# Kernel tuning notes

Measured on AMD Instinct MI355X. Metric: run time of the kernel, lower is better.

## Reference

```python
import jax, jax.numpy as jnp
import numpy as np

B, I, H = 16384, 512, 512
HH = H // 2


def _lrelu(v):
    return jnp.where(v > 0, v, 0.01 * v)


def setup_inputs() -> dict:
    key = jax.random.key(0)
    ks = jax.random.split(key, 20)
    s = 1.0 / np.sqrt(H)
    rn = lambda k, shp, sc: (jax.random.normal(k, shp, jnp.float32) * sc)
    return {
        "x": rn(ks[0], (B, I), 1.0),
        "h0": rn(ks[1], (1, B, H), 1.0),
        "c0": rn(ks[2], (1, B, H), 1.0),
        "cum": jax.random.uniform(ks[3], (B, 1), jnp.float32),
        # LSTM params (torch gate order i, f, g, o)
        "W_ih": rn(ks[4], (4 * H, I), s),
        "W_hh": rn(ks[5], (4 * H, H), s),
        "b_ih": rn(ks[6], (4 * H,), s),
        "b_hh": rn(ks[7], (4 * H,), s),
        # skip gate MLP
        "W_sp": rn(ks[8], (HH, H), s),
        "b_sp": rn(ks[9], (HH,), s),
        "W_sc": rn(ks[10], (HH, H), s),
        "b_sc": rn(ks[11], (HH,), s),
        "W_so": rn(ks[12], (1, HH), s),
        "b_so": rn(ks[13], (1,), s),
        # threshold gate MLP
        "W_tp": rn(ks[14], (HH, H), s),
        "b_tp": rn(ks[15], (HH,), s),
        "W_to": rn(ks[16], (1, HH), s),
        "b_to": rn(ks[17], (1,), s),
    }


def reference(x, h0, c0, cum, W_ih, W_hh, b_ih, b_hh,
              W_sp, b_sp, W_sc, b_sc, W_so, b_so,
              W_tp, b_tp, W_to, b_to):
    # single-step, single-layer LSTM
    gates = x @ W_ih.T + b_ih + h0[0] @ W_hh.T + b_hh  # [B, 4H]
    i_g, f_g, g_g, o_g = jnp.split(gates, 4, axis=-1)
    i_g = jax.nn.sigmoid(i_g)
    f_g = jax.nn.sigmoid(f_g)
    g_g = jnp.tanh(g_g)
    o_g = jax.nn.sigmoid(o_g)
    c1l = f_g * c0[0] + i_g * g_g          # [B, H]
    h1l = o_g * jnp.tanh(c1l)              # [B, H]
    h1, c1 = h1l[None], c1l[None]          # [1, B, H]

    # skip gate: delta prob from c0[-1], c1[-1]
    sg = _lrelu(c0[-1] @ W_sp.T + b_sp + c1[-1] @ W_sc.T + b_sc)  # [B, H/2]
    update_prob_delta = jax.nn.sigmoid(sg @ W_so.T + b_so)        # [B, 1]

    # threshold gate from c0[-1]
    tg = _lrelu(c0[-1] @ W_tp.T + b_tp)                           # [B, H/2]
    update_threshold = jax.nn.sigmoid(tg @ W_to.T + b_to)         # [B, 1]

    update_prob = cum + jnp.minimum(update_prob_delta, 1.0 - cum)  # [B, 1]
    # straight-through round: fwd hard threshold, bwd identity to prob
    hard = (update_prob > update_threshold).astype(jnp.float32)
    update_gate = update_prob + jax.lax.stop_gradient(hard - update_prob)

    new_h = update_gate * h1 + (1.0 - update_gate) * h0  # [1, B, H]
    new_c = update_gate * c1 + (1.0 - update_gate) * c0  # [1, B, H]
    update_cum = (1.0 - update_gate) * update_prob        # [B, 1]
    return (new_h, new_c, update_cum, update_prob_delta, update_prob)
```

## Files before the change

kernel.cpp:

```cpp
#include <hip/hip_runtime.h>
#include <math.h>

#define BB 16384
#define HH 512

typedef short short8 __attribute__((ext_vector_type(8)));
typedef float f32x4 __attribute__((ext_vector_type(4)));
typedef unsigned short ushort_t;

__device__ __forceinline__ float sigm(float v){ return 1.0f/(1.0f+expf(-v)); }

__device__ __forceinline__ unsigned short f2bf(float f){
    unsigned int u = __float_as_uint(f);
    u = u + 0x7FFFu + ((u>>16)&1u);
    return (unsigned short)(u>>16);
}
__device__ __forceinline__ float bf2f(unsigned short h){
    return __uint_as_float(((unsigned int)h)<<16);
}
__device__ __forceinline__ void gll16(const void* g, void* l){
    __builtin_amdgcn_global_load_lds((const __attribute__((address_space(1))) void*)g,
                                     (__attribute__((address_space(3))) void*)l, 16, 0, 0);
}
__device__ __forceinline__ void split_store(float v, ushort_t* ph, ushort_t* pl, int j){
    unsigned short h = f2bf(v);
    unsigned short l = f2bf(v - bf2f(h));
    ph[j] = h; pl[j] = l;
}

__global__ void k_prep_all(
    const float* __restrict__ x, const float* __restrict__ h0, const float* __restrict__ c0,
    const float* __restrict__ W_ih, const float* __restrict__ W_hh,
    const float* __restrict__ b_ih, const float* __restrict__ b_hh,
    const float* __restrict__ W_sp, const float* __restrict__ W_sc, const float* __restrict__ W_tp,
    const float* __restrict__ b_sp, const float* __restrict__ b_sc, const float* __restrict__ b_tp,
    ushort_t* __restrict__ A1h, ushort_t* __restrict__ A1l,
    ushort_t* __restrict__ A2h, ushort_t* __restrict__ A2l,
    ushort_t* __restrict__ B1h, ushort_t* __restrict__ B1l,
    ushort_t* __restrict__ B2h, ushort_t* __restrict__ B2l,
    float* __restrict__ bgp, float* __restrict__ bs2)
{
    int bid = blockIdx.x;
    if (bid < 8192) {
        int u = bid*256 + threadIdx.x;
        int r  = u & 255;
        int c  = (u >> 8) & 3;
        int kt = (u >> 10) & 31;
        int tm = u >> 15;
        int row = tm*256 + r;
        int k0 = kt*32 + c*8;
        const float* src = (k0 < 512) ? (x + (size_t)row*512 + k0)
                                      : (h0 + (size_t)row*512 + (k0-512));
        float4 v0 = *(const float4*)(src);
        float4 v1 = *(const float4*)(src+4);
        float vv[8] = {v0.x,v0.y,v0.z,v0.w,v1.x,v1.y,v1.z,v1.w};
        size_t off = (size_t)u * 8;
#pragma unroll
        for (int j=0;j<8;++j) split_store(vv[j], A1h+off, A1l+off, j);
    } else if (bid < 12288) {
        int u = (bid-8192)*256 + threadIdx.x;
        int r  = u & 127;
        int c  = (u >> 7) & 3;
        int tk = (u >> 9) & 15;
        int tm = u >> 13;
        int row = tm*128 + r;
        int k0 = tk*32 + c*8;
        const float* src = c0 + (size_t)row*512 + k0;
        float4 v0 = *(const float4*)(src);
        float4 v1 = *(const float4*)(src+4);
        float vv[8] = {v0.x,v0.y,v0.z,v0.w,v1.x,v1.y,v1.z,v1.w};
        size_t off = ((size_t)tm*32 + tk)*4096 + (size_t)(c*128 + r)*8;
#pragma unroll
        for (int j=0;j<8;++j) split_store(vv[j], A2h+off, A2l+off, j);
    } else if (bid < 13312) {
        int u = (bid-12288)*256 + threadIdx.x;
        int r  = u & 255;
        int c  = (u >> 8) & 3;
        int kt = (u >> 10) & 31;
        int tn = u >> 15;
        int g = (r>>4)&3;
        int h = tn*64 + (r>>6)*16 + (r&15);
        int wrow = g*512 + h;
        int k0 = kt*32 + c*8;
        const float* src = (k0 < 512) ? (W_ih + (size_t)wrow*512 + k0)
                                      : (W_hh + (size_t)wrow*512 + (k0-512));
        float4 v0 = *(const float4*)(src);
        float4 v1 = *(const float4*)(src+4);
        float vv[8] = {v0.x,v0.y,v0.z,v0.w,v1.x,v1.y,v1.z,v1.w};
        size_t off = (size_t)u * 8;
#pragma unroll
        for (int j=0;j<8;++j) split_store(vv[j], B1h+off, B1l+off, j);
        if (kt == 0 && c == 0) bgp[tn*256 + r] = b_ih[wrow] + b_hh[wrow];
    } else {
        int u = (bid-13312)*256 + threadIdx.x;
        int r  = u & 127;
        int c  = (u >> 7) & 3;
        int tk = (u >> 9) & 31;
        int tn = u >> 14;
        int n = tn*128 + r;
        int k0 = tk*32 + c*8;
        float vv[8];
        if (n < 256) {
            const float* src = (k0 < 512) ? (W_sp + (size_t)n*512 + k0)
                                          : (W_sc + (size_t)n*512 + (k0-512));
            float4 v0 = *(const float4*)(src);
            float4 v1 = *(const float4*)(src+4);
            vv[0]=v0.x; vv[1]=v0.y; vv[2]=v0.z; vv[3]=v0.w;
            vv[4]=v1.x; vv[5]=v1.y; vv[6]=v1.z; vv[7]=v1.w;
        } else if (k0 < 512) {
            const float* src = W_tp + (size_t)(n-256)*512 + k0;
            float4 v0 = *(const float4*)(src);
            float4 v1 = *(const float4*)(src+4);
            vv[0]=v0.x; vv[1]=v0.y; vv[2]=v0.z; vv[3]=v0.w;
            vv[4]=v1.x; vv[5]=v1.y; vv[6]=v1.z; vv[7]=v1.w;
        } else {
#pragma unroll
            for (int j=0;j<8;++j) vv[j] = 0.0f;
        }
        size_t off = (size_t)u * 8;
#pragma unroll
        for (int j=0;j<8;++j) split_store(vv[j], B2h+off, B2l+off, j);
        if (tk == 0 && c == 0) bs2[n] = (n < 256) ? (b_sp[n] + b_sc[n]) : b_tp[n-256];
    }
}

#define GSTEP(T, CA, CB, NA, NB, DO_READS, DO_STAGE, VMASM)                          \
  {                                                                                  \
    if (DO_READS) {                                                                  \
        const ushort_t* bufA1 = &lds[((T)+1) & 3][0];                                \
        const ushort_t* bufB1 = &lds[((T)+1) & 3][8192];                             \
        _Pragma("unroll") for (int f = 0; f < 8; ++f)                                \
            NA[f] = *(const short8*)&bufA1[aoff[f]];                                 \
        _Pragma("unroll") for (int f = 0; f < 4; ++f)                                \
            NB[f] = *(const short8*)&bufB1[boff[f]];                                 \
    }                                                                                \
    if (DO_STAGE) {                                                                  \
        const int uu = (T) + 3;                                                      \
        const ushort_t* As_ = ((uu >> 5) == 1) ? Al : Ah;                            \
        const ushort_t* Bs_ = ((uu >> 5) == 2) ? Bl : Bh;                            \
        size_t ga = ((size_t)tm*32 + (uu & 31))*8192 + (size_t)tid*8;                \
        size_t gb = ((size_t)tn*32 + (uu & 31))*8192 + (size_t)tid*8;                \
        ushort_t* dA = &lds[uu & 3][0];                                              \
        ushort_t* dB = &lds[uu & 3][8192];                                           \
        gll16(As_ + ga,        dA + tid*8);                                          \
        gll16(As_ + ga + 4096, dA + 4096 + tid*8);                                   \
        gll16(Bs_ + gb,        dB + tid*8);                                          \
        gll16(Bs_ + gb + 4096, dB + 4096 + tid*8);                                   \
    }                                                                                \
    __builtin_amdgcn_sched_barrier(0);                                               \
    __builtin_amdgcn_s_setprio(1);                                                   \
    _Pragma("unroll") for (int fm = 0; fm < 8; ++fm)                                 \
        _Pragma("unroll") for (int fn = 0; fn < 4; ++fn)                             \
            acc[fm][fn] = __builtin_amdgcn_mfma_f32_16x16x32_bf16(CA[fm], CB[fn], acc[fm][fn], 0,0,0); \
    __builtin_amdgcn_s_setprio(0);                                                   \
    asm volatile("s_waitcnt lgkmcnt(0)" ::: "memory");                               \
    __builtin_amdgcn_sched_barrier(0);                                               \
    VMASM;                                                                           \
    asm volatile("s_barrier" ::: "memory");                                          \
  }

__global__ __launch_bounds__(512, 2) void k_gemm_gates(
    const ushort_t* __restrict__ Ah, const ushort_t* __restrict__ Al,
    const ushort_t* __restrict__ Bh, const ushort_t* __restrict__ Bl,
    const float* __restrict__ bgp, const float* __restrict__ c0,
    float* __restrict__ outH, float* __restrict__ outC,
    ushort_t* __restrict__ A2h, ushort_t* __restrict__ A2l)
{
    __shared__ __align__(16) ushort_t lds[4][16384];
    const int tid  = threadIdx.x;
    const int lane = tid & 63;
    const int wid  = tid >> 6;
    const int wr   = wid >> 2;
    const int wc   = wid & 3;
    const int l15  = lane & 15;
    const int lq   = lane >> 4;
    const int bid  = (int)blockIdx.x;
    const int v    = (bid & 7)*64 + (bid >> 3);
    const int tm   = v >> 3;
    const int tn   = v & 7;

    f32x4 acc[8][4];
#pragma unroll
    for (int fn = 0; fn < 4; ++fn) {
        float bv = bgp[tn*256 + wc*64 + fn*16 + l15];
#pragma unroll
        for (int fm = 0; fm < 8; ++fm) {
            acc[fm][fn][0]=bv; acc[fm][fn][1]=bv; acc[fm][fn][2]=bv; acc[fm][fn][3]=bv;
        }
    }

    int aoff[8], boff[4];
#pragma unroll
    for (int f = 0; f < 8; ++f) aoff[f] = (lq*256 + wr*128 + f*16 + l15) * 8;
#pragma unroll
    for (int f = 0; f < 4; ++f) boff[f] = (lq*256 + wc*64 + f*16 + l15) * 8;

    short8 a0[8], b0[4], a1[8], b1[4];

#pragma unroll
    for (int u0 = 0; u0 < 3; ++u0) {
        size_t ga = ((size_t)tm*32 + u0)*8192 + (size_t)tid*8;
        size_t gb = ((size_t)tn*32 + u0)*8192 + (size_t)tid*8;
        gll16(Ah + ga,        &lds[u0][0]     + tid*8);
        gll16(Ah + ga + 4096, &lds[u0][4096]  + tid*8);
        gll16(Bh + gb,        &lds[u0][8192]  + tid*8);
        gll16(Bh + gb + 4096, &lds[u0][12288] + tid*8);
    }
    asm volatile("s_waitcnt vmcnt(4)" ::: "memory");
    asm volatile("s_barrier" ::: "memory");
#pragma unroll
    for (int f = 0; f < 8; ++f) a0[f] = *(const short8*)&lds[0][aoff[f]];
#pragma unroll
    for (int f = 0; f < 4; ++f) b0[f] = *(const short8*)&lds[0][8192 + boff[f]];
    asm volatile("s_waitcnt lgkmcnt(0)" ::: "memory");
    __builtin_amdgcn_sched_barrier(0);

    for (int t = 0; t < 92; t += 2) {
        GSTEP(t,   a0, b0, a1, b1, 1, 1, asm volatile("s_waitcnt vmcnt(4)" ::: "memory"));
        GSTEP(t+1, a1, b1, a0, b0, 1, 1, asm volatile("s_waitcnt vmcnt(4)" ::: "memory"));
    }
    GSTEP(92, a0, b0, a1, b1, 1, 1, asm volatile("s_waitcnt vmcnt(4)" ::: "memory"));
    GSTEP(93, a1, b1, a0, b0, 1, 0, asm volatile("s_waitcnt vmcnt(0)" ::: "memory"));
    GSTEP(94, a0, b0, a1, b1, 1, 0, ((void)0));
    GSTEP(95, a1, b1, a0, b0, 0, 0, ((void)0));

    const int h = tn*64 + wc*16 + l15;
#pragma unroll
    for (int fm = 0; fm < 8; ++fm) {
        int row0 = tm*256 + wr*128 + fm*16 + lq*4;
#pragma unroll
        for (int r = 0; r < 4; ++r) {
            int row = row0 + r;
            size_t idx = (size_t)row*512 + h;
            float ig = sigm(acc[fm][0][r]);
            float fg = sigm(acc[fm][1][r]);
            float gg = tanhf(acc[fm][2][r]);
            float og = sigm(acc[fm][3][r]);
            float c1 = fg*c0[idx] + ig*gg;
            float h1 = og*tanhf(c1);
            outC[idx] = c1;
            outH[idx] = h1;
            unsigned short ch = f2bf(c1);
            unsigned short cl = f2bf(c1 - bf2f(ch));
            size_t a2 = ((size_t)(row>>7)*32 + 16 + (h>>5))*4096
                      + (size_t)((((h>>3)&3))*128 + (row&127))*8 + (h&7);
            A2h[a2] = ch;
            A2l[a2] = cl;
        }
    }
}

#define SSTEP(T, CA, CB, NA, NB, DO_READS, DO_STAGE, VMASM)                          \
  {                                                                                  \
    if (DO_READS) {                                                                  \
        const ushort_t* bufA1 = &lds2[((T)+1) & 3][0];                               \
        const ushort_t* bufB1 = &lds2[((T)+1) & 3][4096];                            \
        _Pragma("unroll") for (int f = 0; f < 4; ++f)                                \
            NA[f] = *(const short8*)&bufA1[aoff[f]];                                 \
        _Pragma("unroll") for (int f = 0; f < 4; ++f)                                \
            NB[f] = *(const short8*)&bufB1[boff[f]];                                 \
    }                                                                                \
    if (DO_STAGE) {                                                                  \
        const int uu = (T) + 3;                                                      \
        const ushort_t* As_ = ((uu >> 5) == 1) ? Al : Ah;                            \
        const ushort_t* Bs_ = ((uu >> 5) == 2) ? Bl : Bh;                            \
        size_t ga = ((size_t)tm*32 + (uu & 31))*4096 + (size_t)tid*8;                \
        size_t gb = ((size_t)tn*32 + (uu & 31))*4096 + (size_t)tid*8;                \
        ushort_t* dA = &lds2[uu & 3][0];                                             \
        ushort_t* dB = &lds2[uu & 3][4096];                                          \
        gll16(As_ + ga,        dA + tid*8);                                          \
        gll16(As_ + ga + 2048, dA + 2048 + tid*8);                                   \
        gll16(Bs_ + gb,        dB + tid*8);                                          \
        gll16(Bs_ + gb + 2048, dB + 2048 + tid*8);                                   \
    }                                                                                \
    __builtin_amdgcn_sched_barrier(0);                                               \
    __builtin_amdgcn_s_setprio(1);                                                   \
    _Pragma("unroll") for (int fm = 0; fm < 4; ++fm)                                 \
        _Pragma("unroll") for (int fn = 0; fn < 4; ++fn)                             \
            acc[fm][fn] = __builtin_amdgcn_mfma_f32_16x16x32_bf16(CA[fm], CB[fn], acc[fm][fn], 0,0,0); \
    __builtin_amdgcn_s_setprio(0);                                                   \
    asm volatile("s_waitcnt lgkmcnt(0)" ::: "memory");                               \
    __builtin_amdgcn_sched_barrier(0);                                               \
    VMASM;                                                                           \
    asm volatile("s_barrier" ::: "memory");                                          \
  }

__global__ __launch_bounds__(256, 2) void k_gemm_sgtg(
    const ushort_t* __restrict__ Ah, const ushort_t* __restrict__ Al,
    const ushort_t* __restrict__ Bh, const ushort_t* __restrict__ Bl,
    const float* __restrict__ bs2,
    float* __restrict__ sgtg)
{
    __shared__ __align__(16) ushort_t lds2[4][8192];
    const int tid  = threadIdx.x;
    const int lane = tid & 63;
    const int wid  = tid >> 6;
    const int wr   = wid >> 1;
    const int wc   = wid & 1;
    const int l15  = lane & 15;
    const int lq   = lane >> 4;
    const int bid  = (int)blockIdx.x;
    const int v    = (bid & 7)*64 + (bid >> 3);
    const int tm   = v >> 2;
    const int tn   = v & 3;

    f32x4 acc[4][4];
#pragma unroll
    for (int fn = 0; fn < 4; ++fn) {
        float bv = bs2[tn*128 + wc*64 + fn*16 + l15];
#pragma unroll
        for (int fm = 0; fm < 4; ++fm) {
            acc[fm][fn][0]=bv; acc[fm][fn][1]=bv; acc[fm][fn][2]=bv; acc[fm][fn][3]=bv;
        }
    }

    int aoff[4], boff[4];
#pragma unroll
    for (int f = 0; f < 4; ++f) {
        aoff[f] = (lq*128 + wr*64 + f*16 + l15) * 8;
        boff[f] = (lq*128 + wc*64 + f*16 + l15) * 8;
    }

    short8 a0[4], b0[4], a1[4], b1[4];

#pragma unroll
    for (int u0 = 0; u0 < 3; ++u0) {
        size_t ga = ((size_t)tm*32 + u0)*4096 + (size_t)tid*8;
        size_t gb = ((size_t)tn*32 + u0)*4096 + (size_t)tid*8;
        gll16(Ah + ga,        &lds2[u0][0]    + tid*8);
        gll16(Ah + ga + 2048, &lds2[u0][2048] + tid*8);
        gll16(Bh + gb,        &lds2[u0][4096] + tid*8);
        gll16(Bh + gb + 2048, &lds2[u0][6144] + tid*8);
    }
    asm volatile("s_waitcnt vmcnt(4)" ::: "memory");
    asm volatile("s_barrier" ::: "memory");
#pragma unroll
    for (int f = 0; f < 4; ++f) a0[f] = *(const short8*)&lds2[0][aoff[f]];
#pragma unroll
    for (int f = 0; f < 4; ++f) b0[f] = *(const short8*)&lds2[0][4096 + boff[f]];
    asm volatile("s_waitcnt lgkmcnt(0)" ::: "memory");
    __builtin_amdgcn_sched_barrier(0);

    for (int t = 0; t < 92; t += 2) {
        SSTEP(t,   a0, b0, a1, b1, 1, 1, asm volatile("s_waitcnt vmcnt(4)" ::: "memory"));
        SSTEP(t+1, a1, b1, a0, b0, 1, 1, asm volatile("s_waitcnt vmcnt(4)" ::: "memory"));
    }
    SSTEP(92, a0, b0, a1, b1, 1, 1, asm volatile("s_waitcnt vmcnt(4)" ::: "memory"));
    SSTEP(93, a1, b1, a0, b0, 1, 0, asm volatile("s_waitcnt vmcnt(0)" ::: "memory"));
    SSTEP(94, a0, b0, a1, b1, 1, 0, ((void)0));
    SSTEP(95, a1, b1, a0, b0, 0, 0, ((void)0));

#pragma unroll
    for (int fm = 0; fm < 4; ++fm) {
        int row0 = tm*128 + wr*64 + fm*16 + lq*4;
#pragma unroll
        for (int fn = 0; fn < 4; ++fn) {
            int n = tn*128 + wc*64 + fn*16 + l15;
#pragma unroll
            for (int r = 0; r < 4; ++r) {
                int row = row0 + r;
                float vv = acc[fm][fn][r];
                vv = vv > 0.f ? vv : 0.01f*vv;
                sgtg[(size_t)row*512 + n] = vv;
            }
        }
    }
}

__global__ __launch_bounds__(256) void k_final(
    const float* __restrict__ sgtg,
    const float* __restrict__ h0, const float* __restrict__ c0,
    const float* __restrict__ cum,
    const float* __restrict__ W_so, const float* __restrict__ b_so,
    const float* __restrict__ W_to, const float* __restrict__ b_to,
    float* __restrict__ outH, float* __restrict__ outC,
    float* __restrict__ outCum, float* __restrict__ outDelta, float* __restrict__ outProb)
{
    int w = threadIdx.x >> 6;
    int lane = threadIdx.x & 63;
    int b = blockIdx.x * 4 + w;
    const float* row = sgtg + (size_t)b * 512;
    float so = 0.f, to = 0.f;
#pragma unroll
    for (int u = 0; u < 4; ++u) {
        int c = lane + 64 * u;
        so = fmaf(row[c], W_so[c], so);
        to = fmaf(row[256 + c], W_to[c], to);
    }
#pragma unroll
    for (int off = 32; off; off >>= 1) {
        so += __shfl_down(so, off);
        to += __shfl_down(to, off);
    }
    so = __shfl(so, 0);
    to = __shfl(to, 0);
    float delta = sigm(so + b_so[0]);
    float thr   = sigm(to + b_to[0]);
    float cu = cum[b];
    float prob = cu + fminf(delta, 1.0f - cu);
    float hard = (prob > thr) ? 1.0f : 0.0f;
    if (lane == 0) {
        outDelta[b] = delta;
        outProb[b]  = prob;
        outCum[b]   = (1.0f - hard) * prob;
    }
    if (hard == 0.0f) {
#pragma unroll
        for (int u = 0; u < 8; ++u) {
            size_t idx = (size_t)b * 512 + lane + 64 * u;
            outH[idx] = h0[idx];
            outC[idx] = c0[idx];
        }
    }
}

extern "C" void kernel_launch(void* const* d_in, const int* in_sizes, int n_in,
                              void* d_out, int out_size, void* d_ws, size_t ws_size,
                              hipStream_t stream)
{
    const float* x    = (const float*)d_in[0];
    const float* h0   = (const float*)d_in[1];
    const float* c0   = (const float*)d_in[2];
    const float* cum  = (const float*)d_in[3];
    const float* W_ih = (const float*)d_in[4];
    const float* W_hh = (const float*)d_in[5];
    const float* b_ih = (const float*)d_in[6];
    const float* b_hh = (const float*)d_in[7];
    const float* W_sp = (const float*)d_in[8];
    const float* b_sp = (const float*)d_in[9];
    const float* W_sc = (const float*)d_in[10];
    const float* b_sc = (const float*)d_in[11];
    const float* W_so = (const float*)d_in[12];
    const float* b_so = (const float*)d_in[13];
    const float* W_tp = (const float*)d_in[14];
    const float* b_tp = (const float*)d_in[15];
    const float* W_to = (const float*)d_in[16];
    const float* b_to = (const float*)d_in[17];

    float* out      = (float*)d_out;
    float* outH     = out;
    float* outC     = out + (size_t)BB * HH;
    float* outCum   = out + (size_t)2 * BB * HH;
    float* outDelta = outCum + BB;
    float* outProb  = outDelta + BB;

    char* w = (char*)d_ws;
    ushort_t* A1h = (ushort_t*)(w);
    ushort_t* A1l = (ushort_t*)(w + 33554432ull);
    ushort_t* A2h = (ushort_t*)(w + 67108864ull);
    ushort_t* A2l = (ushort_t*)(w + 100663296ull);
    ushort_t* B1h = (ushort_t*)(w + 134217728ull);
    ushort_t* B1l = (ushort_t*)(w + 138412032ull);
    ushort_t* B2h = (ushort_t*)(w + 142606336ull);
    ushort_t* B2l = (ushort_t*)(w + 143654912ull);
    float*    bgp = (float*)(w + 144703488ull);
    float*    bs2 = (float*)(w + 144711680ull);
    float*    sgtg = (float*)A1h;

    k_prep_all<<<13568, 256, 0, stream>>>(x, h0, c0, W_ih, W_hh, b_ih, b_hh,
                                          W_sp, W_sc, W_tp, b_sp, b_sc, b_tp,
                                          A1h, A1l, A2h, A2l, B1h, B1l, B2h, B2l,
                                          bgp, bs2);
    k_gemm_gates<<<512, 512, 0, stream>>>(A1h, A1l, B1h, B1l, bgp, c0,
                                          outH, outC, A2h, A2l);
    k_gemm_sgtg<<<512, 256, 0, stream>>>(A2h, A2l, B2h, B2l, bs2, sgtg);
    k_final<<<4096, 256, 0, stream>>>(sgtg, h0, c0, cum, W_so, b_so, W_to, b_to,
                                      outH, outC, outCum, outDelta, outProb);
}
```

Baseline: 340.0 us.

## Load A operand directly from global in MFMA fragment layout, stage only B in LDS

```diff
diff --git a/kernel.cpp b/kernel.cpp
--- a/kernel.cpp
+++ b/kernel.cpp
@@ -43,12 +43,14 @@
     int bid = blockIdx.x;
     if (bid < 8192) {
         int u = bid*256 + threadIdx.x;
-        int r  = u & 255;
-        int c  = (u >> 8) & 3;
-        int kt = (u >> 10) & 31;
-        int tm = u >> 15;
-        int row = tm*256 + r;
-        int k0 = kt*32 + c*8;
+        int tm  = u >> 14;
+        int rem = u & 16383;
+        int kt  = rem >> 9;
+        int lq  = (rem >> 7) & 3;
+        int f   = (rem >> 4) & 7;
+        int l15 = rem & 15;
+        int row = tm*128 + f*16 + l15;
+        int k0  = kt*32 + lq*8;
         const float* src = (k0 < 512) ? (x + (size_t)row*512 + k0)
                                       : (h0 + (size_t)row*512 + (k0-512));
         float4 v0 = *(const float4*)(src);
@@ -59,17 +61,19 @@
         for (int j=0;j<8;++j) split_store(vv[j], A1h+off, A1l+off, j);
     } else if (bid < 12288) {
         int u = (bid-8192)*256 + threadIdx.x;
-        int r  = u & 127;
-        int c  = (u >> 7) & 3;
-        int tk = (u >> 9) & 15;
-        int tm = u >> 13;
-        int row = tm*128 + r;
-        int k0 = tk*32 + c*8;
+        int tm  = u >> 13;
+        int rem = u & 8191;
+        int kt  = rem >> 9;
+        int lq  = (rem >> 7) & 3;
+        int f   = (rem >> 4) & 7;
+        int l15 = rem & 15;
+        int row = tm*128 + f*16 + l15;
+        int k0  = kt*32 + lq*8;
         const float* src = c0 + (size_t)row*512 + k0;
         float4 v0 = *(const float4*)(src);
         float4 v1 = *(const float4*)(src+4);
         float vv[8] = {v0.x,v0.y,v0.z,v0.w,v1.x,v1.y,v1.z,v1.w};
-        size_t off = ((size_t)tm*32 + tk)*4096 + (size_t)(c*128 + r)*8;
+        size_t off = ((size_t)tm*32 + kt)*4096 + (size_t)(rem & 511)*8;
 #pragma unroll
         for (int j=0;j<8;++j) split_store(vv[j], A2h+off, A2l+off, j);
     } else if (bid < 13312) {
@@ -124,60 +128,57 @@
     }
 }
 
-#define GSTEP(T, CA, CB, NA, NB, DO_READS, DO_STAGE, VMASM)                          \
+#define GSTEP(T, CA, CB, NA, NB, DO_A, DO_BSTAGE, DO_BREAD, WAITASM)                 \
   {                                                                                  \
-    if (DO_READS) {                                                                  \
-        const ushort_t* bufA1 = &lds[((T)+1) & 3][0];                                \
-        const ushort_t* bufB1 = &lds[((T)+1) & 3][8192];                             \
+    if (DO_A) {                                                                      \
+        const int un = (T) + 1;                                                      \
+        const ushort_t* As_ = ((un >> 5) == 1) ? Al : Ah;                            \
+        const ushort_t* ap = As_ + ((size_t)tm*32 + (un & 31))*4096 + aG;            \
         _Pragma("unroll") for (int f = 0; f < 8; ++f)                                \
-            NA[f] = *(const short8*)&bufA1[aoff[f]];                                 \
-        _Pragma("unroll") for (int f = 0; f < 4; ++f)                                \
-            NB[f] = *(const short8*)&bufB1[boff[f]];                                 \
-    }                                                                                \
-    if (DO_STAGE) {                                                                  \
+            NA[f] = *(const short8*)(ap + f*128);                                    \
+    }                                                                                \
+    if (DO_BSTAGE) {                                                                 \
         const int uu = (T) + 3;                                                      \
-        const ushort_t* As_ = ((uu >> 5) == 1) ? Al : Ah;                            \
         const ushort_t* Bs_ = ((uu >> 5) == 2) ? Bl : Bh;                            \
-        size_t ga = ((size_t)tm*32 + (uu & 31))*8192 + (size_t)tid*8;                \
-        size_t gb = ((size_t)tn*32 + (uu & 31))*8192 + (size_t)tid*8;                \
-        ushort_t* dA = &lds[uu & 3][0];                                              \
-        ushort_t* dB = &lds[uu & 3][8192];                                           \
-        gll16(As_ + ga,        dA + tid*8);                                          \
-        gll16(As_ + ga + 4096, dA + 4096 + tid*8);                                   \
-        gll16(Bs_ + gb,        dB + tid*8);                                          \
-        gll16(Bs_ + gb + 4096, dB + 4096 + tid*8);                                   \
-    }                                                                                \
-    __builtin_amdgcn_sched_barrier(0);                                               \
+        const ushort_t* gB = Bs_ + ((size_t)tn*32 + (uu & 31))*8192;                 \
+        ushort_t* dB = &ldsB[uu & 3][0];                                             \
+        _Pragma("unroll") for (int q = 0; q < 4; ++q)                                \
+            gll16(gB + (q*256 + tid)*8, dB + (q*256 + tid)*8);                       \
+    }                                                                                \
+    if (DO_BREAD) {                                                                  \
+        const ushort_t* bB = &ldsB[((T)+1) & 3][0];                                  \
+        _Pragma("unroll") for (int fn = 0; fn < 4; ++fn)                             \
+            NB[fn] = *(const short8*)&bB[boff[fn]];                                  \
+    }                                                                                \
     __builtin_amdgcn_s_setprio(1);                                                   \
     _Pragma("unroll") for (int fm = 0; fm < 8; ++fm)                                 \
         _Pragma("unroll") for (int fn = 0; fn < 4; ++fn)                             \
             acc[fm][fn] = __builtin_amdgcn_mfma_f32_16x16x32_bf16(CA[fm], CB[fn], acc[fm][fn], 0,0,0); \
     __builtin_amdgcn_s_setprio(0);                                                   \
-    asm volatile("s_waitcnt lgkmcnt(0)" ::: "memory");                               \
     __builtin_amdgcn_sched_barrier(0);                                               \
-    VMASM;                                                                           \
+    WAITASM;                                                                         \
+    __builtin_amdgcn_sched_barrier(0);                                               \
     asm volatile("s_barrier" ::: "memory");                                          \
   }
 
-__global__ __launch_bounds__(512, 2) void k_gemm_gates(
+__global__ __launch_bounds__(256, 2) void k_gemm_gates(
     const ushort_t* __restrict__ Ah, const ushort_t* __restrict__ Al,
     const ushort_t* __restrict__ Bh, const ushort_t* __restrict__ Bl,
     const float* __restrict__ bgp, const float* __restrict__ c0,
     float* __restrict__ outH, float* __restrict__ outC,
     ushort_t* __restrict__ A2h, ushort_t* __restrict__ A2l)
 {
-    __shared__ __align__(16) ushort_t lds[4][16384];
+    __shared__ __align__(16) ushort_t ldsB[4][8192];
     const int tid  = threadIdx.x;
     const int lane = tid & 63;
-    const int wid  = tid >> 6;
-    const int wr   = wid >> 2;
-    const int wc   = wid & 3;
+    const int wc   = tid >> 6;
     const int l15  = lane & 15;
     const int lq   = lane >> 4;
     const int bid  = (int)blockIdx.x;
-    const int v    = (bid & 7)*64 + (bid >> 3);
+    const int v    = (bid & 7)*128 + (bid >> 3);
     const int tm   = v >> 3;
     const int tn   = v & 7;
+    const int aG   = lq*1024 + l15*8;
 
     f32x4 acc[8][4];
 #pragma unroll
@@ -189,45 +190,44 @@
         }
     }
 
-    int aoff[8], boff[4];
-#pragma unroll
-    for (int f = 0; f < 8; ++f) aoff[f] = (lq*256 + wr*128 + f*16 + l15) * 8;
+    int boff[4];
 #pragma unroll
     for (int f = 0; f < 4; ++f) boff[f] = (lq*256 + wc*64 + f*16 + l15) * 8;
 
     short8 a0[8], b0[4], a1[8], b1[4];
 
-#pragma unroll
-    for (int u0 = 0; u0 < 3; ++u0) {
-        size_t ga = ((size_t)tm*32 + u0)*8192 + (size_t)tid*8;
-        size_t gb = ((size_t)tn*32 + u0)*8192 + (size_t)tid*8;
-        gll16(Ah + ga,        &lds[u0][0]     + tid*8);
-        gll16(Ah + ga + 4096, &lds[u0][4096]  + tid*8);
-        gll16(Bh + gb,        &lds[u0][8192]  + tid*8);
-        gll16(Bh + gb + 4096, &lds[u0][12288] + tid*8);
+    {
+        const ushort_t* ap0 = Ah + (size_t)tm*32*4096 + aG;
+#pragma unroll
+        for (int f = 0; f < 8; ++f) a0[f] = *(const short8*)(ap0 + f*128);
+#pragma unroll
+        for (int u0 = 0; u0 < 3; ++u0) {
+            const ushort_t* gB = Bh + ((size_t)tn*32 + u0)*8192;
+#pragma unroll
+            for (int q = 0; q < 4; ++q)
+                gll16(gB + (q*256 + tid)*8, &ldsB[u0][(q*256 + tid)*8]);
+        }
     }
     asm volatile("s_waitcnt vmcnt(4)" ::: "memory");
     asm volatile("s_barrier" ::: "memory");
 #pragma unroll
-    for (int f = 0; f < 8; ++f) a0[f] = *(const short8*)&lds[0][aoff[f]];
-#pragma unroll
-    for (int f = 0; f < 4; ++f) b0[f] = *(const short8*)&lds[0][8192 + boff[f]];
+    for (int f = 0; f < 4; ++f) b0[f] = *(const short8*)&ldsB[0][boff[f]];
     asm volatile("s_waitcnt lgkmcnt(0)" ::: "memory");
     __builtin_amdgcn_sched_barrier(0);
 
     for (int t = 0; t < 92; t += 2) {
-        GSTEP(t,   a0, b0, a1, b1, 1, 1, asm volatile("s_waitcnt vmcnt(4)" ::: "memory"));
-        GSTEP(t+1, a1, b1, a0, b0, 1, 1, asm volatile("s_waitcnt vmcnt(4)" ::: "memory"));
-    }
-    GSTEP(92, a0, b0, a1, b1, 1, 1, asm volatile("s_waitcnt vmcnt(4)" ::: "memory"));
-    GSTEP(93, a1, b1, a0, b0, 1, 0, asm volatile("s_waitcnt vmcnt(0)" ::: "memory"));
-    GSTEP(94, a0, b0, a1, b1, 1, 0, ((void)0));
-    GSTEP(95, a1, b1, a0, b0, 0, 0, ((void)0));
+        GSTEP(t,   a0,b0, a1,b1, 1,1,1, asm volatile("s_waitcnt vmcnt(4) lgkmcnt(0)" ::: "memory"));
+        GSTEP(t+1, a1,b1, a0,b0, 1,1,1, asm volatile("s_waitcnt vmcnt(4) lgkmcnt(0)" ::: "memory"));
+    }
+    GSTEP(92, a0,b0, a1,b1, 1,1,1, asm volatile("s_waitcnt vmcnt(4) lgkmcnt(0)" ::: "memory"));
+    GSTEP(93, a1,b1, a0,b0, 1,0,1, asm volatile("s_waitcnt vmcnt(0) lgkmcnt(0)" ::: "memory"));
+    GSTEP(94, a0,b0, a1,b1, 1,0,1, asm volatile("s_waitcnt vmcnt(0) lgkmcnt(0)" ::: "memory"));
+    GSTEP(95, a1,b1, a0,b0, 0,0,0, ((void)0));
 
     const int h = tn*64 + wc*16 + l15;
 #pragma unroll
     for (int fm = 0; fm < 8; ++fm) {
-        int row0 = tm*256 + wr*128 + fm*16 + lq*4;
+        int row0 = tm*128 + fm*16 + lq*4;
 #pragma unroll
         for (int r = 0; r < 4; ++r) {
             int row = row0 + r;
@@ -243,119 +243,115 @@
             unsigned short ch = f2bf(c1);
             unsigned short cl = f2bf(c1 - bf2f(ch));
             size_t a2 = ((size_t)(row>>7)*32 + 16 + (h>>5))*4096
-                      + (size_t)((((h>>3)&3))*128 + (row&127))*8 + (h&7);
+                      + (size_t)((h>>3)&3)*1024 + (size_t)(((row&127)>>4))*128
+                      + (size_t)(row&15)*8 + (h&7);
             A2h[a2] = ch;
             A2l[a2] = cl;
         }
     }
 }
 
-#define SSTEP(T, CA, CB, NA, NB, DO_READS, DO_STAGE, VMASM)                          \
+#define SSTEP(T, CA, CB, NA, NB, DO_A, DO_BSTAGE, DO_BREAD, WAITASM)                 \
   {                                                                                  \
-    if (DO_READS) {                                                                  \
-        const ushort_t* bufA1 = &lds2[((T)+1) & 3][0];                               \
-        const ushort_t* bufB1 = &lds2[((T)+1) & 3][4096];                            \
-        _Pragma("unroll") for (int f = 0; f < 4; ++f)                                \
-            NA[f] = *(const short8*)&bufA1[aoff[f]];                                 \
-        _Pragma("unroll") for (int f = 0; f < 4; ++f)                                \
-            NB[f] = *(const short8*)&bufB1[boff[f]];                                 \
-    }                                                                                \
-    if (DO_STAGE) {                                                                  \
+    if (DO_A) {                                                                      \
+        const int un = (T) + 1;                                                      \
+        const ushort_t* As_ = ((un >> 5) == 1) ? Al : Ah;                            \
+        const ushort_t* ap = As_ + ((size_t)tm*32 + (un & 31))*4096 + aG;            \
+        _Pragma("unroll") for (int f = 0; f < 8; ++f)                                \
+            NA[f] = *(const short8*)(ap + f*128);                                    \
+    }                                                                                \
+    if (DO_BSTAGE) {                                                                 \
         const int uu = (T) + 3;                                                      \
-        const ushort_t* As_ = ((uu >> 5) == 1) ? Al : Ah;                            \
         const ushort_t* Bs_ = ((uu >> 5) == 2) ? Bl : Bh;                            \
-        size_t ga = ((size_t)tm*32 + (uu & 31))*4096 + (size_t)tid*8;                \
-        size_t gb = ((size_t)tn*32 + (uu & 31))*4096 + (size_t)tid*8;                \
-        ushort_t* dA = &lds2[uu & 3][0];                                             \
-        ushort_t* dB = &lds2[uu & 3][4096];                                          \
-        gll16(As_ + ga,        dA + tid*8);                                          \
-        gll16(As_ + ga + 2048, dA + 2048 + tid*8);                                   \
-        gll16(Bs_ + gb,        dB + tid*8);                                          \
-        gll16(Bs_ + gb + 2048, dB + 2048 + tid*8);                                   \
-    }                                                                                \
-    __builtin_amdgcn_sched_barrier(0);                                               \
+        const ushort_t* gB = Bs_ + ((size_t)tn*32 + (uu & 31))*4096;                 \
+        ushort_t* dB = &ldsB2[uu & 3][0];                                            \
+        _Pragma("unroll") for (int q = 0; q < 2; ++q)                                \
+            gll16(gB + (q*256 + tid)*8, dB + (q*256 + tid)*8);                       \
+    }                                                                                \
+    if (DO_BREAD) {                                                                  \
+        const ushort_t* bB = &ldsB2[((T)+1) & 3][0];                                 \
+        _Pragma("unroll") for (int fn = 0; fn < 2; ++fn)                             \
+            NB[fn] = *(const short8*)&bB[boff2[fn]];                                 \
+    }                                                                                \
     __builtin_amdgcn_s_setprio(1);                                                   \
-    _Pragma("unroll") for (int fm = 0; fm < 4; ++fm)                                 \
-        _Pragma("unroll") for (int fn = 0; fn < 4; ++fn)                             \
+    _Pragma("unroll") for (int fm = 0; fm < 8; ++fm)                                 \
+        _Pragma("unroll") for (int fn = 0; fn < 2; ++fn)                             \
             acc[fm][fn] = __builtin_amdgcn_mfma_f32_16x16x32_bf16(CA[fm], CB[fn], acc[fm][fn], 0,0,0); \
     __builtin_amdgcn_s_setprio(0);                                                   \
-    asm volatile("s_waitcnt lgkmcnt(0)" ::: "memory");                               \
     __builtin_amdgcn_sched_barrier(0);                                               \
-    VMASM;                                                                           \
+    WAITASM;                                                                         \
+    __builtin_amdgcn_sched_barrier(0);                                               \
     asm volatile("s_barrier" ::: "memory");                                          \
   }
 
-__global__ __launch_bounds__(256, 2) void k_gemm_sgtg(
+__global__ __launch_bounds__(256, 3) void k_gemm_sgtg(
     const ushort_t* __restrict__ Ah, const ushort_t* __restrict__ Al,
     const ushort_t* __restrict__ Bh, const ushort_t* __restrict__ Bl,
     const float* __restrict__ bs2,
     float* __restrict__ sgtg)
 {
-    __shared__ __align__(16) ushort_t lds2[4][8192];
+    __shared__ __align__(16) ushort_t ldsB2[4][4096];
     const int tid  = threadIdx.x;
     const int lane = tid & 63;
-    const int wid  = tid >> 6;
-    const int wr   = wid >> 1;
-    const int wc   = wid & 1;
+    const int wc   = tid >> 6;
     const int l15  = lane & 15;
     const int lq   = lane >> 4;
     const int bid  = (int)blockIdx.x;
     const int v    = (bid & 7)*64 + (bid >> 3);
     const int tm   = v >> 2;
     const int tn   = v & 3;
-
-    f32x4 acc[4][4];
-#pragma unroll
-    for (int fn = 0; fn < 4; ++fn) {
-        float bv = bs2[tn*128 + wc*64 + fn*16 + l15];
-#pragma unroll
-        for (int fm = 0; fm < 4; ++fm) {
+    const int aG   = lq*1024 + l15*8;
+
+    f32x4 acc[8][2];
+#pragma unroll
+    for (int fn = 0; fn < 2; ++fn) {
+        float bv = bs2[tn*128 + wc*32 + fn*16 + l15];
+#pragma unroll
+        for (int fm = 0; fm < 8; ++fm) {
             acc[fm][fn][0]=bv; acc[fm][fn][1]=bv; acc[fm][fn][2]=bv; acc[fm][fn][3]=bv;
         }
     }
 
-    int aoff[4], boff[4];
-#pragma unroll
-    for (int f = 0; f < 4; ++f) {
-        aoff[f] = (lq*128 + wr*64 + f*16 + l15) * 8;
-        boff[f] = (lq*128 + wc*64 + f*16 + l15) * 8;
-    }
-
-    short8 a0[4], b0[4], a1[4], b1[4];
-
-#pragma unroll
-    for (int u0 = 0; u0 < 3; ++u0) {
-        size_t ga = ((size_t)tm*32 + u0)*4096 + (size_t)tid*8;
-        size_t gb = ((size_t)tn*32 + u0)*4096 + (size_t)tid*8;
-        gll16(Ah + ga,        &lds2[u0][0]    + tid*8);
-        gll16(Ah + ga + 2048, &lds2[u0][2048] + tid*8);
-        gll16(Bh + gb,        &lds2[u0][4096] + tid*8);
-        gll16(Bh + gb + 2048, &lds2[u0][6144] + tid*8);
-    }
-    asm volatile("s_waitcnt vmcnt(4)" ::: "memory");
+    int boff2[2];
+#pragma unroll
+    for (int f = 0; f < 2; ++f) boff2[f] = (lq*128 + wc*32 + f*16 + l15) * 8;
+
+    short8 a0[8], b0[2], a1[8], b1[2];
+
+    {
+        const ushort_t* ap0 = Ah + (size_t)tm*32*4096 + aG;
+#pragma unroll
+        for (int f = 0; f < 8; ++f) a0[f] = *(const short8*)(ap0 + f*128);
+#pragma unroll
+        for (int u0 = 0; u0 < 3; ++u0) {
+            const ushort_t* gB = Bh + ((size_t)tn*32 + u0)*4096;
+#pragma unroll
+            for (int q = 0; q < 2; ++q)
+                gll16(gB + (q*256 + tid)*8, &ldsB2[u0][(q*256 + tid)*8]);
+        }
+    }
+    asm volatile("s_waitcnt vmcnt(2)" ::: "memory");
     asm volatile("s_barrier" ::: "memory");
 #pragma unroll
-    for (int f = 0; f < 4; ++f) a0[f] = *(const short8*)&lds2[0][aoff[f]];
-#pragma unroll
-    for (int f = 0; f < 4; ++f) b0[f] = *(const short8*)&lds2[0][4096 + boff[f]];
+    for (int f = 0; f < 2; ++f) b0[f] = *(const short8*)&ldsB2[0][boff2[f]];
     asm volatile("s_waitcnt lgkmcnt(0)" ::: "memory");
     __builtin_amdgcn_sched_barrier(0);
 
     for (int t = 0; t < 92; t += 2) {
-        SSTEP(t,   a0, b0, a1, b1, 1, 1, asm volatile("s_waitcnt vmcnt(4)" ::: "memory"));
-        SSTEP(t+1, a1, b1, a0, b0, 1, 1, asm volatile("s_waitcnt vmcnt(4)" ::: "memory"));
-    }
-    SSTEP(92, a0, b0, a1, b1, 1, 1, asm volatile("s_waitcnt vmcnt(4)" ::: "memory"));
-    SSTEP(93, a1, b1, a0, b0, 1, 0, asm volatile("s_waitcnt vmcnt(0)" ::: "memory"));
-    SSTEP(94, a0, b0, a1, b1, 1, 0, ((void)0));
-    SSTEP(95, a1, b1, a0, b0, 0, 0, ((void)0));
-
-#pragma unroll
-    for (int fm = 0; fm < 4; ++fm) {
-        int row0 = tm*128 + wr*64 + fm*16 + lq*4;
-#pragma unroll
-        for (int fn = 0; fn < 4; ++fn) {
-            int n = tn*128 + wc*64 + fn*16 + l15;
+        SSTEP(t,   a0,b0, a1,b1, 1,1,1, asm volatile("s_waitcnt vmcnt(2) lgkmcnt(0)" ::: "memory"));
+        SSTEP(t+1, a1,b1, a0,b0, 1,1,1, asm volatile("s_waitcnt vmcnt(2) lgkmcnt(0)" ::: "memory"));
+    }
+    SSTEP(92, a0,b0, a1,b1, 1,1,1, asm volatile("s_waitcnt vmcnt(2) lgkmcnt(0)" ::: "memory"));
+    SSTEP(93, a1,b1, a0,b0, 1,0,1, asm volatile("s_waitcnt vmcnt(0) lgkmcnt(0)" ::: "memory"));
+    SSTEP(94, a0,b0, a1,b1, 1,0,1, asm volatile("s_waitcnt vmcnt(0) lgkmcnt(0)" ::: "memory"));
+    SSTEP(95, a1,b1, a0,b0, 0,0,0, ((void)0));
+
+#pragma unroll
+    for (int fm = 0; fm < 8; ++fm) {
+        int row0 = tm*128 + fm*16 + lq*4;
+#pragma unroll
+        for (int fn = 0; fn < 2; ++fn) {
+            int n = tn*128 + wc*32 + fn*16 + l15;
 #pragma unroll
             for (int r = 0; r < 4; ++r) {
                 int row = row0 + r;
@@ -461,8 +457,8 @@
                                           W_sp, W_sc, W_tp, b_sp, b_sc, b_tp,
                                           A1h, A1l, A2h, A2l, B1h, B1l, B2h, B2l,
                                           bgp, bs2);
-    k_gemm_gates<<<512, 512, 0, stream>>>(A1h, A1l, B1h, B1l, bgp, c0,
-                                          outH, outC, A2h, A2l);
+    k_gemm_gates<<<1024, 256, 0, stream>>>(A1h, A1l, B1h, B1l, bgp, c0,
+                                           outH, outC, A2h, A2l);
     k_gemm_sgtg<<<512, 256, 0, stream>>>(A2h, A2l, B2h, B2l, bs2, sgtg);
     k_final<<<4096, 256, 0, stream>>>(sgtg, h0, c0, cum, W_so, b_so, W_to, b_to,
                                       outH, outC, outCum, outDelta, outProb);
```

New measurement: 383.5 us. +12.8%, slower.

## Shrink gates GEMM tile to 256x128 with 256 threads and 3-stage LDS ring

Applied to the files above, without the earlier changes.

```diff
diff --git a/kernel.cpp b/kernel.cpp
--- a/kernel.cpp
+++ b/kernel.cpp
@@ -74,12 +74,12 @@
         for (int j=0;j<8;++j) split_store(vv[j], A2h+off, A2l+off, j);
     } else if (bid < 13312) {
         int u = (bid-12288)*256 + threadIdx.x;
-        int r  = u & 255;
-        int c  = (u >> 8) & 3;
-        int kt = (u >> 10) & 31;
-        int tn = u >> 15;
-        int g = (r>>4)&3;
-        int h = tn*64 + (r>>6)*16 + (r&15);
+        int col = u & 127;
+        int c  = (u >> 7) & 3;
+        int kt = (u >> 9) & 31;
+        int tn = u >> 14;
+        int g = (col>>4)&3;
+        int h = tn*32 + (col>>6)*16 + (col&15);
         int wrow = g*512 + h;
         int k0 = kt*32 + c*8;
         const float* src = (k0 < 512) ? (W_ih + (size_t)wrow*512 + k0)
@@ -90,7 +90,7 @@
         size_t off = (size_t)u * 8;
 #pragma unroll
         for (int j=0;j<8;++j) split_store(vv[j], B1h+off, B1l+off, j);
-        if (kt == 0 && c == 0) bgp[tn*256 + r] = b_ih[wrow] + b_hh[wrow];
+        if (kt == 0 && c == 0) bgp[tn*128 + col] = b_ih[wrow] + b_hh[wrow];
     } else {
         int u = (bid-13312)*256 + threadIdx.x;
         int r  = u & 127;
@@ -124,28 +124,28 @@
     }
 }
 
-#define GSTEP(T, CA, CB, NA, NB, DO_READS, DO_STAGE, VMASM)                          \
+#define GSTEP(K, CA, CB, NA, NB, BR, BS, DO_READS, DO_STAGE, WAITASM)                \
   {                                                                                  \
-    if (DO_READS) {                                                                  \
-        const ushort_t* bufA1 = &lds[((T)+1) & 3][0];                                \
-        const ushort_t* bufB1 = &lds[((T)+1) & 3][8192];                             \
-        _Pragma("unroll") for (int f = 0; f < 8; ++f)                                \
-            NA[f] = *(const short8*)&bufA1[aoff[f]];                                 \
-        _Pragma("unroll") for (int f = 0; f < 4; ++f)                                \
-            NB[f] = *(const short8*)&bufB1[boff[f]];                                 \
-    }                                                                                \
     if (DO_STAGE) {                                                                  \
-        const int uu = (T) + 3;                                                      \
+        const int uu = (K) + 2;                                                      \
         const ushort_t* As_ = ((uu >> 5) == 1) ? Al : Ah;                            \
         const ushort_t* Bs_ = ((uu >> 5) == 2) ? Bl : Bh;                            \
-        size_t ga = ((size_t)tm*32 + (uu & 31))*8192 + (size_t)tid*8;                \
-        size_t gb = ((size_t)tn*32 + (uu & 31))*8192 + (size_t)tid*8;                \
-        ushort_t* dA = &lds[uu & 3][0];                                              \
-        ushort_t* dB = &lds[uu & 3][8192];                                           \
-        gll16(As_ + ga,        dA + tid*8);                                          \
-        gll16(As_ + ga + 4096, dA + 4096 + tid*8);                                   \
-        gll16(Bs_ + gb,        dB + tid*8);                                          \
-        gll16(Bs_ + gb + 4096, dB + 4096 + tid*8);                                   \
+        const ushort_t* gA = As_ + ((size_t)tm*32 + (uu & 31))*8192;                 \
+        const ushort_t* gB = Bs_ + ((size_t)tn*32 + (uu & 31))*4096;                 \
+        ushort_t* dA = &lds[(BS)][0];                                                \
+        ushort_t* dB = &lds[(BS)][8192];                                             \
+        _Pragma("unroll") for (int q = 0; q < 4; ++q)                                \
+            gll16(gA + (q*256 + tid)*8, dA + (q*256 + tid)*8);                       \
+        _Pragma("unroll") for (int q = 0; q < 2; ++q)                                \
+            gll16(gB + (q*256 + tid)*8, dB + (q*256 + tid)*8);                       \
+    }                                                                                \
+    if (DO_READS) {                                                                  \
+        const ushort_t* bA = &lds[(BR)][0];                                          \
+        const ushort_t* bB = &lds[(BR)][8192];                                       \
+        _Pragma("unroll") for (int f = 0; f < 8; ++f)                                \
+            NA[f] = *(const short8*)&bA[aoff[f]];                                    \
+        _Pragma("unroll") for (int f = 0; f < 4; ++f)                                \
+            NB[f] = *(const short8*)&bB[boff[f]];                                    \
     }                                                                                \
     __builtin_amdgcn_sched_barrier(0);                                               \
     __builtin_amdgcn_s_setprio(1);                                                   \
@@ -155,34 +155,36 @@
     __builtin_amdgcn_s_setprio(0);                                                   \
     asm volatile("s_waitcnt lgkmcnt(0)" ::: "memory");                               \
     __builtin_amdgcn_sched_barrier(0);                                               \
-    VMASM;                                                                           \
+    WAITASM;                                                                         \
+    __builtin_amdgcn_sched_barrier(0);                                               \
     asm volatile("s_barrier" ::: "memory");                                          \
   }
-
-__global__ __launch_bounds__(512, 2) void k_gemm_gates(
+#define VM0 asm volatile("s_waitcnt vmcnt(0)" ::: "memory")
+
+__global__ __launch_bounds__(256, 2) void k_gemm_gates(
     const ushort_t* __restrict__ Ah, const ushort_t* __restrict__ Al,
     const ushort_t* __restrict__ Bh, const ushort_t* __restrict__ Bl,
     const float* __restrict__ bgp, const float* __restrict__ c0,
     float* __restrict__ outH, float* __restrict__ outC,
     ushort_t* __restrict__ A2h, ushort_t* __restrict__ A2l)
 {
-    __shared__ __align__(16) ushort_t lds[4][16384];
+    __shared__ __align__(16) ushort_t lds[3][12288];
     const int tid  = threadIdx.x;
     const int lane = tid & 63;
     const int wid  = tid >> 6;
-    const int wr   = wid >> 2;
-    const int wc   = wid & 3;
+    const int wr   = wid >> 1;
+    const int wc   = wid & 1;
     const int l15  = lane & 15;
     const int lq   = lane >> 4;
     const int bid  = (int)blockIdx.x;
-    const int v    = (bid & 7)*64 + (bid >> 3);
-    const int tm   = v >> 3;
-    const int tn   = v & 7;
+    const int v    = (bid & 7)*128 + (bid >> 3);
+    const int tm   = v >> 4;
+    const int tn   = v & 15;
 
     f32x4 acc[8][4];
 #pragma unroll
     for (int fn = 0; fn < 4; ++fn) {
-        float bv = bgp[tn*256 + wc*64 + fn*16 + l15];
+        float bv = bgp[tn*128 + wc*64 + fn*16 + l15];
 #pragma unroll
         for (int fm = 0; fm < 8; ++fm) {
             acc[fm][fn][0]=bv; acc[fm][fn][1]=bv; acc[fm][fn][2]=bv; acc[fm][fn][3]=bv;
@@ -193,20 +195,22 @@
 #pragma unroll
     for (int f = 0; f < 8; ++f) aoff[f] = (lq*256 + wr*128 + f*16 + l15) * 8;
 #pragma unroll
-    for (int f = 0; f < 4; ++f) boff[f] = (lq*256 + wc*64 + f*16 + l15) * 8;
+    for (int f = 0; f < 4; ++f) boff[f] = (lq*128 + wc*64 + f*16 + l15) * 8;
 
     short8 a0[8], b0[4], a1[8], b1[4];
 
 #pragma unroll
-    for (int u0 = 0; u0 < 3; ++u0) {
-        size_t ga = ((size_t)tm*32 + u0)*8192 + (size_t)tid*8;
-        size_t gb = ((size_t)tn*32 + u0)*8192 + (size_t)tid*8;
-        gll16(Ah + ga,        &lds[u0][0]     + tid*8);
-        gll16(Ah + ga + 4096, &lds[u0][4096]  + tid*8);
-        gll16(Bh + gb,        &lds[u0][8192]  + tid*8);
-        gll16(Bh + gb + 4096, &lds[u0][12288] + tid*8);
-    }
-    asm volatile("s_waitcnt vmcnt(4)" ::: "memory");
+    for (int u0 = 0; u0 < 2; ++u0) {
+        const ushort_t* gA = Ah + ((size_t)tm*32 + u0)*8192;
+        const ushort_t* gB = Bh + ((size_t)tn*32 + u0)*4096;
+#pragma unroll
+        for (int q = 0; q < 4; ++q)
+            gll16(gA + (q*256 + tid)*8, &lds[u0][(q*256 + tid)*8]);
+#pragma unroll
+        for (int q = 0; q < 2; ++q)
+            gll16(gB + (q*256 + tid)*8, &lds[u0][8192 + (q*256 + tid)*8]);
+    }
+    asm volatile("s_waitcnt vmcnt(0)" ::: "memory");
     asm volatile("s_barrier" ::: "memory");
 #pragma unroll
     for (int f = 0; f < 8; ++f) a0[f] = *(const short8*)&lds[0][aoff[f]];
@@ -215,16 +219,22 @@
     asm volatile("s_waitcnt lgkmcnt(0)" ::: "memory");
     __builtin_amdgcn_sched_barrier(0);
 
-    for (int t = 0; t < 92; t += 2) {
-        GSTEP(t,   a0, b0, a1, b1, 1, 1, asm volatile("s_waitcnt vmcnt(4)" ::: "memory"));
-        GSTEP(t+1, a1, b1, a0, b0, 1, 1, asm volatile("s_waitcnt vmcnt(4)" ::: "memory"));
-    }
-    GSTEP(92, a0, b0, a1, b1, 1, 1, asm volatile("s_waitcnt vmcnt(4)" ::: "memory"));
-    GSTEP(93, a1, b1, a0, b0, 1, 0, asm volatile("s_waitcnt vmcnt(0)" ::: "memory"));
-    GSTEP(94, a0, b0, a1, b1, 1, 0, ((void)0));
-    GSTEP(95, a1, b1, a0, b0, 0, 0, ((void)0));
-
-    const int h = tn*64 + wc*16 + l15;
+    for (int t = 0; t < 90; t += 6) {
+        GSTEP(t+0, a0,b0, a1,b1, 1,2, 1,1, VM0);
+        GSTEP(t+1, a1,b1, a0,b0, 2,0, 1,1, VM0);
+        GSTEP(t+2, a0,b0, a1,b1, 0,1, 1,1, VM0);
+        GSTEP(t+3, a1,b1, a0,b0, 1,2, 1,1, VM0);
+        GSTEP(t+4, a0,b0, a1,b1, 2,0, 1,1, VM0);
+        GSTEP(t+5, a1,b1, a0,b0, 0,1, 1,1, VM0);
+    }
+    GSTEP(90, a0,b0, a1,b1, 1,2, 1,1, VM0);
+    GSTEP(91, a1,b1, a0,b0, 2,0, 1,1, VM0);
+    GSTEP(92, a0,b0, a1,b1, 0,1, 1,1, VM0);
+    GSTEP(93, a1,b1, a0,b0, 1,2, 1,1, VM0);
+    GSTEP(94, a0,b0, a1,b1, 2,0, 1,0, VM0);
+    GSTEP(95, a1,b1, a0,b0, 0,0, 0,0, ((void)0));
+
+    const int h = tn*32 + wc*16 + l15;
 #pragma unroll
     for (int fm = 0; fm < 8; ++fm) {
         int row0 = tm*256 + wr*128 + fm*16 + lq*4;
@@ -461,8 +471,8 @@
                                           W_sp, W_sc, W_tp, b_sp, b_sc, b_tp,
                                           A1h, A1l, A2h, A2l, B1h, B1l, B2h, B2l,
                                           bgp, bs2);
-    k_gemm_gates<<<512, 512, 0, stream>>>(A1h, A1l, B1h, B1l, bgp, c0,
-                                          outH, outC, A2h, A2l);
+    k_gemm_gates<<<1024, 256, 0, stream>>>(A1h, A1l, B1h, B1l, bgp, c0,
+                                           outH, outC, A2h, A2l);
     k_gemm_sgtg<<<512, 256, 0, stream>>>(A2h, A2l, B2h, B2l, bs2, sgtg);
     k_final<<<4096, 256, 0, stream>>>(sgtg, h0, c0, cum, W_so, b_so, W_to, b_to,
                                       outH, outC, outCum, outDelta, outProb);
```

After: 343.0 us. Within noise of the previous version (+0.9%).
